# Optimization experiments

Measured on AMD Instinct MI355X. Metric: run time of the kernel, lower is better.

The kernel has to match this reference:

```python
import jax, jax.numpy as jnp
import numpy as np

# dims: P planes, N planar nodes/plane, M nexus nodes, E edges/plane, C classes
P, N, M, E, C, FP, FN = 3, 100000, 30000, 200000, 5, 64, 32


def class_linear(x, W, b):
    # x: [..., C, in], W: [C, out, in], b: [C, out] -> [..., C, out]
    return jnp.einsum('...ci,coi->...co', x, W) + b


def setup_inputs() -> dict:
    key = jax.random.key(0)
    ks = jax.random.split(key, 12)
    def nrm(k, shape, scale=1.0):
        return jax.random.normal(k, shape, jnp.float32) * scale
    return {
        'x': nrm(ks[0], (P, N, C, FP)),
        'nexus': nrm(ks[1], (M, C, FN)),
        'edge_src': jax.random.randint(ks[2], (P, E), 0, N, jnp.int32),
        'edge_dst': jax.random.randint(ks[3], (P, E), 0, M, jnp.int32),
        'Wn1': nrm(ks[4], (C, FN, P * FP), (P * FP) ** -0.5),
        'bn1': jnp.zeros((C, FN), jnp.float32),
        'Wn2': nrm(ks[5], (C, FN, FN), FN ** -0.5),
        'bn2': jnp.zeros((C, FN), jnp.float32),
        'We': nrm(ks[6], (P, C, 1, FP + FN), (FP + FN) ** -0.5),
        'be': jnp.zeros((P, C, 1), jnp.float32),
        'Wd1': nrm(ks[7], (P, C, FP, FP + FN), (FP + FN) ** -0.5),
        'bd1': jnp.zeros((P, C, FP), jnp.float32),
        'Wd2': nrm(ks[8], (P, C, FP, FP), FP ** -0.5),
        'bd2': jnp.zeros((P, C, FP), jnp.float32),
    }


def reference(x, nexus, edge_src, edge_dst, Wn1, bn1, Wn2, bn2,
              We, be, Wd1, bd1, Wd2, bd2):
    # --- nexus_up: SimpleConv (sum-aggregate planar features at nexus nodes) ---
    def up_one(xp, src, dst):
        return jax.ops.segment_sum(xp[src], dst, num_segments=M)  # [M,C,FP]
    up = jax.vmap(up_one)(x, edge_src, edge_dst)                   # [P,M,C,FP]
    # torch.cat(n, dim=-1) over planes -> [M, C, P*FP]
    n_cat = jnp.transpose(up, (1, 2, 0, 3)).reshape(M, C, P * FP)

    # --- nexus_net: ClassLinear -> tanh -> ClassLinear -> tanh ---
    n = jnp.tanh(class_linear(n_cat, Wn1, bn1))
    n = jnp.tanh(class_linear(n, Wn2, bn2))                        # [M,C,FN]

    # --- nexus_down per plane (flow target_to_source, aggr mean at src) ---
    def down_one(xp, src, dst, We_p, be_p, W1, b1, W2, b2):
        x_i = xp[src]                                              # [E,C,FP]
        n_j = n[dst]                                               # [E,C,FN]
        feat = jax.lax.stop_gradient(jnp.concatenate([x_i, n_j], -1))
        # per-class scalar logit, softmax over class dim (dim=1)
        w = jax.nn.softmax(class_linear(feat, We_p, be_p), axis=1)  # [E,C,1]
        msg = w * n_j                                               # [E,C,FN]
        s = jax.ops.segment_sum(msg, src, num_segments=N)           # [N,C,FN]
        cnt = jax.ops.segment_sum(jnp.ones((E,), msg.dtype), src, num_segments=N)
        aggr = s / jnp.maximum(cnt, 1.0)[:, None, None]             # scatter-mean
        h = jnp.tanh(class_linear(jnp.concatenate([xp, aggr], -1), W1, b1))
        return jnp.tanh(class_linear(h, W2, b2))                    # [N,C,FP]

    out = jax.vmap(down_one)(x, edge_src, edge_dst, We, be, Wd1, bd1, Wd2, bd2)
    return out  # [P,N,C,FP] updated planar embeddings (x['u'],x['v'],x['y'])
```

## Files before the change

### kernel.cpp

```cpp
#include <hip/hip_runtime.h>
#include <hip/hip_fp16.h>

#define P_ 3
#define N_ 100000
#define M_ 30000
#define E_ 200000
#define C_ 5
#define FP_ 64
#define FN_ 32
#define PFP_ 192
#define FPFN_ 96
#define PE_ 600000
#define PN_ 300000
#define PM_ 90000
#define NT_ 32
#define XSP_ 324
#define TILES_ ((N_ + NT_ - 1) / NT_)
#define NTD_ 64
#define TILESD_ ((N_ + NTD_ - 1) / NTD_)
#define CFN_ 160
#define NW1_ 92160
#define NW2_ 61440
#define NB_S_ ((PN_ + 1023) / 1024)
#define NB_D_ ((PM_ + 1023) / 1024)
#define NB_CNT_ ((PE_ + 255) / 256)
#define NB_WC_ ((NW1_ + 255) / 256)
#define NB_PROJ_ (P_ * TILES_)
#define NB_FILL_ ((PE_ + 319) / 320)

typedef _Float16 f16x8 __attribute__((ext_vector_type(8)));
typedef float f32x4 __attribute__((ext_vector_type(4)));

__device__ __forceinline__ float fast_tanh(float v) {
  float x = fminf(fmaxf(v, -15.0f), 15.0f);
  float t = __expf(2.0f * x);
  return __fdividef(t - 1.0f, t + 1.0f);
}

__device__ __forceinline__ f16x8 ld8(const __half* p) {
  return *(const f16x8*)(const void*)p;
}

__global__ void k_countw(const int* __restrict__ esrc, const int* __restrict__ edst,
                         int* __restrict__ cnt_src, int* __restrict__ cnt_dst,
                         const float* __restrict__ Wd1, const float* __restrict__ Wd2,
                         __half* __restrict__ w1h, __half* __restrict__ w2h) {
  int b = blockIdx.x;
  if (b < NB_CNT_) {
    int i = b * 256 + threadIdx.x;
    if (i >= PE_) return;
    int p = i / E_;
    atomicAdd(&cnt_src[p * N_ + esrc[i]], 1);
    atomicAdd(&cnt_dst[p * M_ + edst[i]], 1);
  } else {
    int i = (b - NB_CNT_) * 256 + threadIdx.x;
    if (i < NW1_) w1h[i] = __float2half(Wd1[i]);
    if (i < NW2_) w2h[i] = __float2half(Wd2[i]);
  }
}

__global__ void k_scan1c(const int* __restrict__ in_s, int* __restrict__ out_s,
                         int* __restrict__ aux_s,
                         const int* __restrict__ in_d, int* __restrict__ out_d,
                         int* __restrict__ aux_d) {
  __shared__ int lds[256];
  int b = blockIdx.x, t = threadIdx.x;
  const int* in;
  int* out;
  int* aux;
  int n;
  if (b < NB_S_) { in = in_s; out = out_s; aux = aux_s; n = PN_; }
  else           { b -= NB_S_; in = in_d; out = out_d; aux = aux_d; n = PM_; }
  int base = b * 1024 + t * 4;
  int v0 = (base + 0 < n) ? in[base + 0] : 0;
  int v1 = (base + 1 < n) ? in[base + 1] : 0;
  int v2 = (base + 2 < n) ? in[base + 2] : 0;
  int v3 = (base + 3 < n) ? in[base + 3] : 0;
  lds[t] = v0 + v1 + v2 + v3;
  __syncthreads();
  for (int off = 1; off < 256; off <<= 1) {
    int xv = (t >= off) ? lds[t - off] : 0;
    __syncthreads();
    lds[t] += xv;
    __syncthreads();
  }
  if (t == 255) aux[b] = lds[255];
  int run = (t == 0) ? 0 : lds[t - 1];
  if (base + 0 < n) out[base + 0] = run; run += v0;
  if (base + 1 < n) out[base + 1] = run; run += v1;
  if (base + 2 < n) out[base + 2] = run; run += v2;
  if (base + 3 < n) out[base + 3] = run;
}

__global__ void k_scan2c(int* __restrict__ aux_s, int* __restrict__ end_s,
                         int* __restrict__ aux_d, int* __restrict__ end_d) {
  __shared__ int lds[1024];
  int t = threadIdx.x;
  int* aux = (blockIdx.x == 0) ? aux_s : aux_d;
  int* offe = (blockIdx.x == 0) ? end_s : end_d;
  int nb = (blockIdx.x == 0) ? NB_S_ : NB_D_;
  lds[t] = (t < nb) ? aux[t] : 0;
  __syncthreads();
  for (int off = 1; off < 1024; off <<= 1) {
    int xv = (t >= off) ? lds[t - off] : 0;
    __syncthreads();
    lds[t] += xv;
    __syncthreads();
  }
  if (t < nb) aux[t] = (t == 0) ? 0 : lds[t - 1];
  if (t == 0) offe[0] = lds[nb - 1];
}

__global__ void k_scan3c(int* __restrict__ off_s, const int* __restrict__ aux_s,
                         int* __restrict__ cur_s,
                         int* __restrict__ off_d, const int* __restrict__ aux_d,
                         int* __restrict__ cur_d) {
  int i = blockIdx.x * 256 + threadIdx.x;
  if (i < PN_) {
    int v = off_s[i] + aux_s[i >> 10];
    off_s[i] = v;
    cur_s[i] = v;
  } else if (i < PN_ + PM_) {
    int j = i - PN_;
    int v = off_d[j] + aux_d[j >> 10];
    off_d[j] = v;
    cur_d[j] = v;
  }
}

__global__ __launch_bounds__(320) void k_projfill(
    const float* __restrict__ x, const float* __restrict__ Wn1,
    const float* __restrict__ We,
    __half* __restrict__ y, float* __restrict__ xdot,
    __half* __restrict__ xh, int write_xh,
    const int* __restrict__ esrc, const int* __restrict__ edst,
    int* __restrict__ cur_src, int* __restrict__ cur_dst,
    int* __restrict__ list_src, int* __restrict__ list_src_e,
    int* __restrict__ list_dst, int* __restrict__ list_dst_e) {
  __shared__ __align__(16) __half xs[NT_ * XSP_];
  int bp = blockIdx.x;
  int t = threadIdx.x;

  if (bp >= NB_PROJ_) {
    int i = (bp - NB_PROJ_) * 320 + t;
    if (i < PE_) {
      int p = i / E_;
      int s = esrc[i], d = edst[i];
      int ps = atomicAdd(&cur_src[p * N_ + s], 1);
      list_src[ps] = d;
      list_src_e[ps] = i;
      int pd = atomicAdd(&cur_dst[p * M_ + d], 1);
      list_dst[pd] = s;
      list_dst_e[pd] = i;
    }
    return;
  }

  int p = bp / TILES_, tile = bp % TILES_;
  int base = tile * NT_;
  int rows = min(NT_, N_ - base);
  int g = t / CFN_, u = t % CFN_;
  int c = u >> 5;

  __half2 w[32];
  {
    const float* wr = &Wn1[(size_t)u * PFP_ + p * FP_];
    #pragma unroll
    for (int i = 0; i < 32; ++i) w[i] = __floats2half2_rn(wr[2*i], wr[2*i+1]);
  }

  const float* xb = x + (size_t)(p * N_ + base) * 320;
  __half* xo = xh + (size_t)(p * N_ + base) * 320;
  int chunks = rows * 40;
  for (int idx = t; idx < chunks; idx += 320) {
    int row = idx / 40, col = idx % 40;
    const float4* s4 = (const float4*)&xb[row * 320 + col * 8];
    float4 v0 = s4[0], v1 = s4[1];
    union { __half2 h[4]; float4 f; } u4;
    u4.h[0] = __floats2half2_rn(v0.x, v0.y);
    u4.h[1] = __floats2half2_rn(v0.z, v0.w);
    u4.h[2] = __floats2half2_rn(v1.x, v1.y);
    u4.h[3] = __floats2half2_rn(v1.z, v1.w);
    __half2* d = (__half2*)&xs[row * XSP_ + col * 8];
    d[0] = u4.h[0]; d[1] = u4.h[1]; d[2] = u4.h[2]; d[3] = u4.h[3];
    if (write_xh) *(float4*)&xo[row * 320 + col * 8] = u4.f;
  }
  __syncthreads();

  for (int r = g; r < rows; r += 2) {
    const __half2* xr = (const __half2*)&xs[r * XSP_ + c * FP_];
    __half2 acc = __floats2half2_rn(0.f, 0.f);
    #pragma unroll
    for (int i = 0; i < 32; ++i) acc = __hfma2(xr[i], w[i], acc);
    float s = __low2float(acc) + __high2float(acc);
    y[(size_t)(p * N_ + base + r) * CFN_ + u] = __float2half(s);
  }

  {
    int cx = t >> 6, nodex = t & 63;
    if (nodex < rows) {
      const __half2* xr = (const __half2*)&xs[nodex * XSP_ + cx * FP_];
      const float2* wer = (const float2*)&We[(p * C_ + cx) * FPFN_];
      float s = 0.f;
      #pragma unroll
      for (int i = 0; i < 32; ++i) {
        float2 wv = wer[i];
        __half2 xv = xr[i];
        s += __low2float(xv) * wv.x + __high2float(xv) * wv.y;
      }
      xdot[(size_t)(p * N_ + base + nodex) * C_ + cx] = s;
    }
  }
}

__global__ __launch_bounds__(320) void k_nexus(
    const __half* __restrict__ y,
    const int* __restrict__ off_dst, const int* __restrict__ list_dst,
    const int* __restrict__ list_dst_e, const int* __restrict__ esrc,
    const float* __restrict__ bn1,
    const float* __restrict__ Wn2, const float* __restrict__ bn2,
    const float* __restrict__ We,
    const float* __restrict__ xdot, const float* __restrict__ be,
    __half* __restrict__ nout, __half* __restrict__ wbuf) {
  __shared__ float part[4][CFN_];
  __shared__ __align__(16) float h1S[CFN_];
  __shared__ __align__(16) float h2S[CFN_];
  __shared__ float ndS[P_ * C_];
  __shared__ float beS[P_ * C_];
  int m = blockIdx.x;
  int t = threadIdx.x;
  int g = t / 80, u2 = t % 80;

  float afx = 0.f, afy = 0.f;
  #pragma unroll
  for (int p = 0; p < P_; ++p) {
    int o0 = off_dst[p * M_ + m];
    int o1 = off_dst[p * M_ + m + 1];
    const __half2* yp2 = (const __half2*)(y + (size_t)p * N_ * CFN_);
    for (int e0 = o0 + g; e0 < o1; e0 += 8) {
      int e1 = e0 + 4;
      int s0 = list_dst[e0];
      int s1 = list_dst[e1 < o1 ? e1 : e0];
      __half2 v0 = yp2[(size_t)s0 * 80 + u2];
      __half2 v1 = yp2[(size_t)s1 * 80 + u2];
      afx += __low2float(v0); afy += __high2float(v0);
      if (e1 < o1) { afx += __low2float(v1); afy += __high2float(v1); }
    }
  }
  part[g][2 * u2]     = afx;
  part[g][2 * u2 + 1] = afy;
  __syncthreads();
  if (t < CFN_) {
    float pre = part[0][t] + part[1][t] + part[2][t] + part[3][t] + bn1[t];
    h1S[t] = fast_tanh(pre);
  }
  __syncthreads();
  if (t < CFN_) {
    int c = t >> 5;
    const float4* f4 = (const float4*)&h1S[c * FN_];
    const float4* w4 = (const float4*)&Wn2[(size_t)t * FN_];
    float a = bn2[t];
    #pragma unroll
    for (int i = 0; i < FN_ / 4; ++i) {
      float4 f = f4[i], wv = w4[i];
      a += f.x * wv.x + f.y * wv.y + f.z * wv.z + f.w * wv.w;
    }
    float nv = fast_tanh(a);
    h2S[t] = nv;
    nout[(size_t)m * CFN_ + t] = __float2half(nv);
  }
  __syncthreads();
  if (t < P_ * C_) {
    int p = t / C_, cc = t % C_;
    const float* wv = &We[(p * C_ + cc) * FPFN_ + FP_];
    float a = 0.f;
    #pragma unroll
    for (int j = 0; j < FN_; ++j) a += h2S[cc * FN_ + j] * wv[j];
    ndS[t] = a;
    beS[t] = be[t];
  }
  __syncthreads();
  #pragma unroll
  for (int p = 0; p < P_; ++p) {
    int o0 = off_dst[p * M_ + m];
    int o1 = off_dst[p * M_ + m + 1];
    for (int e = o0 + t; e < o1; e += 320) {
      int i = list_dst_e[e];
      int src = esrc[i];
      const float* xd = &xdot[(size_t)(p * N_ + src) * C_];
      float lg[C_];
      #pragma unroll
      for (int cc = 0; cc < C_; ++cc) lg[cc] = xd[cc] + ndS[p * C_ + cc] + beS[p * C_ + cc];
      float mx = fmaxf(fmaxf(fmaxf(lg[0], lg[1]), fmaxf(lg[2], lg[3])), lg[4]);
      float s = 0.f;
      #pragma unroll
      for (int cc = 0; cc < C_; ++cc) { lg[cc] = __expf(lg[cc] - mx); s += lg[cc]; }
      float inv = __fdividef(1.0f, s);
      __half* wp = &wbuf[(size_t)i * C_];
      #pragma unroll
      for (int cc = 0; cc < C_; ++cc) wp[cc] = __float2half(lg[cc] * inv);
    }
  }
}

template<int XH>
__global__ __launch_bounds__(128, 6) void k_dec(
    const float* __restrict__ x, const __half* __restrict__ xh,
    const __half* __restrict__ nout, const __half* __restrict__ wbuf,
    const int* __restrict__ off_src, const int* __restrict__ list_src,
    const int* __restrict__ list_src_e,
    const __half* __restrict__ w1h, const float* __restrict__ bd1,
    const __half* __restrict__ w2h, const float* __restrict__ bd2,
    float* __restrict__ out) {
  __shared__ __align__(16) __half featS[NTD_ * 104];

  int bp = blockIdx.x;
  int pc = bp / TILESD_;
  int tile = bp % TILESD_;
  int p = pc / C_, c = pc % C_;
  int base = tile * NTD_;
  int rows = min(NTD_, N_ - base);

  int t = threadIdx.x;
  int w = t >> 6, l = t & 63;
  int l15 = l & 15, l4 = l >> 4;

  if constexpr (XH) {
    for (int idx = t; idx < NTD_ * 8; idx += 128) {
      int node = idx >> 3, q = idx & 7;
      if (node < rows) {
        float4 v = *(const float4*)&xh[(size_t)(p * N_ + base + node) * 320 + c * 64 + q * 8];
        *(float4*)&featS[node * 104 + q * 8] = v;
      }
    }
  } else {
    for (int idx = t; idx < NTD_ * 16; idx += 128) {
      int node = idx >> 4, fq = idx & 15;
      if (node < rows) {
        float4 v = *(const float4*)&x[(size_t)(p * N_ + base + node) * 320 + c * 64 + fq * 4];
        __half2* dst = (__half2*)&featS[node * 104 + fq * 4];
        dst[0] = __floats2half2_rn(v.x, v.y);
        dst[1] = __floats2half2_rn(v.z, v.w);
      }
    }
  }
  {
    int nd = t >> 1, hf = t & 1;
    if (nd < rows) {
      int pn = p * N_ + base + nd;
      int o0 = off_src[pn], o1 = off_src[pn + 1];
      float acc[16];
      #pragma unroll
      for (int i = 0; i < 16; ++i) acc[i] = 0.f;
      for (int e = o0; e < o1; e += 2) {
        int e1 = e + 1;
        bool has1 = (e1 < o1);
        int d0 = list_src[e];
        int i0 = list_src_e[e];
        int d1 = list_src[has1 ? e1 : e];
        int i1 = list_src_e[has1 ? e1 : e];
        float wg0 = __half2float(wbuf[(size_t)i0 * C_ + c]);
        float wg1 = __half2float(wbuf[(size_t)i1 * C_ + c]);
        const __half2* nr0 = (const __half2*)&nout[(size_t)d0 * CFN_ + c * FN_ + hf * 16];
        const __half2* nr1 = (const __half2*)&nout[(size_t)d1 * CFN_ + c * FN_ + hf * 16];
        __half2 v0[8], v1[8];
        #pragma unroll
        for (int i = 0; i < 8; ++i) v0[i] = nr0[i];
        #pragma unroll
        for (int i = 0; i < 8; ++i) v1[i] = nr1[i];
        #pragma unroll
        for (int i = 0; i < 8; ++i) {
          acc[2 * i]     += wg0 * __low2float(v0[i]);
          acc[2 * i + 1] += wg0 * __high2float(v0[i]);
        }
        if (has1) {
          #pragma unroll
          for (int i = 0; i < 8; ++i) {
            acc[2 * i]     += wg1 * __low2float(v1[i]);
            acc[2 * i + 1] += wg1 * __high2float(v1[i]);
          }
        }
      }
      float invd = __fdividef(1.0f, fmaxf((float)(o1 - o0), 1.0f));
      __half2* dst2 = (__half2*)&featS[nd * 104 + 64 + hf * 16];
      #pragma unroll
      for (int i = 0; i < 8; ++i)
        dst2[i] = __floats2half2_rn(acc[2 * i] * invd, acc[2 * i + 1] * invd);
    }
  }
  __syncthreads();

  int rbase = w * 32;
  const __half* w1g = w1h + (size_t)(p * C_ + c) * 64 * 96;
  const __half* w2g = w2h + (size_t)(p * C_ + c) * 64 * 64;

  f32x4 acc[2][4];
  #pragma unroll
  for (int tt = 0; tt < 4; ++tt) {
    float bv = bd1[(p * C_ + c) * FP_ + tt * 16 + l15];
    #pragma unroll
    for (int rt = 0; rt < 2; ++rt) acc[rt][tt] = (f32x4){bv, bv, bv, bv};
  }
  #pragma unroll
  for (int s = 0; s < 3; ++s) {
    f16x8 a0 = ld8(&featS[(rbase + l15) * 104 + s * 32 + l4 * 8]);
    f16x8 a1 = ld8(&featS[(rbase + 16 + l15) * 104 + s * 32 + l4 * 8]);
    #pragma unroll
    for (int tt = 0; tt < 4; ++tt) {
      f16x8 b = ld8(&w1g[(tt * 16 + l15) * 96 + s * 32 + l4 * 8]);
      acc[0][tt] = __builtin_amdgcn_mfma_f32_16x16x32_f16(a0, b, acc[0][tt], 0, 0, 0);
      acc[1][tt] = __builtin_amdgcn_mfma_f32_16x16x32_f16(a1, b, acc[1][tt], 0, 0, 0);
    }
  }
  #pragma unroll
  for (int rt = 0; rt < 2; ++rt)
    #pragma unroll
    for (int tt = 0; tt < 4; ++tt) {
      #pragma unroll
      for (int r = 0; r < 4; ++r) {
        int nrow = rbase + rt * 16 + l4 * 4 + r;
        featS[nrow * 104 + tt * 16 + l15] = __float2half(fast_tanh(acc[rt][tt][r]));
      }
    }

  f32x4 acc2[2][4];
  #pragma unroll
  for (int tt = 0; tt < 4; ++tt) {
    float bv = bd2[(p * C_ + c) * FP_ + tt * 16 + l15];
    #pragma unroll
    for (int rt = 0; rt < 2; ++rt) acc2[rt][tt] = (f32x4){bv, bv, bv, bv};
  }
  #pragma unroll
  for (int s = 0; s < 2; ++s) {
    f16x8 a0 = ld8(&featS[(rbase + l15) * 104 + s * 32 + l4 * 8]);
    f16x8 a1 = ld8(&featS[(rbase + 16 + l15) * 104 + s * 32 + l4 * 8]);
    #pragma unroll
    for (int tt = 0; tt < 4; ++tt) {
      f16x8 b = ld8(&w2g[(tt * 16 + l15) * 64 + s * 32 + l4 * 8]);
      acc2[0][tt] = __builtin_amdgcn_mfma_f32_16x16x32_f16(a0, b, acc2[0][tt], 0, 0, 0);
      acc2[1][tt] = __builtin_amdgcn_mfma_f32_16x16x32_f16(a1, b, acc2[1][tt], 0, 0, 0);
    }
  }
  #pragma unroll
  for (int rt = 0; rt < 2; ++rt)
    #pragma unroll
    for (int tt = 0; tt < 4; ++tt) {
      #pragma unroll
      for (int r = 0; r < 4; ++r) {
        int nrow = rbase + rt * 16 + l4 * 4 + r;
        int node = base + nrow;
        if (node < N_) {
          out[(size_t)(p * N_ + node) * 320 + c * 64 + tt * 16 + l15] =
              fast_tanh(acc2[rt][tt][r]);
        }
      }
    }
}

#define WS_Y      0ll
#define WS_NOUT   24000000ll
#define WS_LISTSE 26400000ll
#define WS_WBUF   27000000ll
#define WS_XDOT   28800000ll
#define WS_OFFS   30750000ll
#define WS_OFFD   31050001ll
#define WS_CURS   31140002ll
#define WS_CURD   31440002ll
#define WS_LISTS  31530002ll
#define WS_LISTD  32130002ll
#define WS_AUX1   32730002ll
#define WS_AUX2   32730514ll
#define WS_W1H    32731026ll
#define WS_W2H    32777106ll
#define WS_LISTDE 32808000ll
#define WS_XH     33408000ll
#define WS_XH_END_BYTES ((WS_XH + 48000000ll) * 4ll)

extern "C" void kernel_launch(void* const* d_in, const int* in_sizes, int n_in,
                              void* d_out, int out_size, void* d_ws, size_t ws_size,
                              hipStream_t stream) {
  const float* x   = (const float*)d_in[0];
  const int* esrc  = (const int*)d_in[2];
  const int* edst  = (const int*)d_in[3];
  const float* Wn1 = (const float*)d_in[4];
  const float* bn1 = (const float*)d_in[5];
  const float* Wn2 = (const float*)d_in[6];
  const float* bn2 = (const float*)d_in[7];
  const float* We  = (const float*)d_in[8];
  const float* be  = (const float*)d_in[9];
  const float* Wd1 = (const float*)d_in[10];
  const float* bd1 = (const float*)d_in[11];
  const float* Wd2 = (const float*)d_in[12];
  const float* bd2 = (const float*)d_in[13];
  float* out = (float*)d_out;

  float* wsf = (float*)d_ws;
  int*   wsi = (int*)d_ws;
  __half* ybuf = (__half*)d_ws;
  __half* nout = (__half*)(wsi + WS_NOUT);
  __half* wbuf = (__half*)(wsi + WS_WBUF);
  float* xdot = wsf + WS_XDOT;
  int* off_src = wsi + WS_OFFS;
  int* off_dst = wsi + WS_OFFD;
  int* cur_src = wsi + WS_CURS;
  int* cur_dst = wsi + WS_CURD;
  int* list_src = wsi + WS_LISTS;
  int* list_src_e = wsi + WS_LISTSE;
  int* list_dst = wsi + WS_LISTD;
  int* list_dst_e = wsi + WS_LISTDE;
  int* aux1 = wsi + WS_AUX1;
  int* aux2 = wsi + WS_AUX2;
  __half* w1h = (__half*)(wsi + WS_W1H);
  __half* w2h = (__half*)(wsi + WS_W2H);
  __half* xh  = (__half*)(wsi + WS_XH);

  int use_xh = (ws_size >= (size_t)WS_XH_END_BYTES) ? 1 : 0;

  hipMemsetAsync(cur_src, 0, (PN_ + PM_) * sizeof(int), stream);
  k_countw<<<NB_CNT_ + NB_WC_, 256, 0, stream>>>(esrc, edst, cur_src, cur_dst,
                                                 Wd1, Wd2, w1h, w2h);
  k_scan1c<<<NB_S_ + NB_D_, 256, 0, stream>>>(cur_src, off_src, aux1,
                                              cur_dst, off_dst, aux2);
  k_scan2c<<<2, 1024, 0, stream>>>(aux1, off_src + PN_, aux2, off_dst + PM_);
  k_scan3c<<<(PN_ + PM_ + 255) / 256, 256, 0, stream>>>(off_src, aux1, cur_src,
                                                        off_dst, aux2, cur_dst);

  k_projfill<<<NB_PROJ_ + NB_FILL_, 320, 0, stream>>>(
      x, Wn1, We, ybuf, xdot, xh, use_xh,
      esrc, edst, cur_src, cur_dst,
      list_src, list_src_e, list_dst, list_dst_e);

  k_nexus<<<M_, 320, 0, stream>>>(ybuf, off_dst, list_dst, list_dst_e, esrc,
                                  bn1, Wn2, bn2, We, xdot, be, nout, wbuf);

  if (use_xh) {
    k_dec<1><<<P_ * C_ * TILESD_, 128, 0, stream>>>(x, xh, nout, wbuf,
                                                    off_src, list_src, list_src_e,
                                                    w1h, bd1, w2h, bd2, out);
  } else {
    k_dec<0><<<P_ * C_ * TILESD_, 128, 0, stream>>>(x, xh, nout, wbuf,
                                                    off_src, list_src, list_src_e,
                                                    w1h, bd1, w2h, bd2, out);
  }
}
```

Before: 868.0 us.

## Use MFMA for nexus input projection with swizzled LDS tile and fp16 Wn1

Replaces the per-thread packed-half dot products in the projection kernel with 16x16x32 fp16 MFMA instructions. The tile grows to 64 nodes with 256 threads, and the LDS tile switches from a padded stride to an XOR swizzle. Wn1 is pre-converted to fp16 in the weight-conversion kernel so MFMA can load B fragments directly. The aim is to cut VALU work and register pressure in the projection and to gain fp32 accumulation. The cost is a new workspace region and a shift of the xh workspace offset.

```diff
diff --git a/kernel.cpp b/kernel.cpp
--- a/kernel.cpp
+++ b/kernel.cpp
@@ -13,20 +13,20 @@
 #define PE_ 600000
 #define PN_ 300000
 #define PM_ 90000
-#define NT_ 32
-#define XSP_ 324
+#define NT_ 64
 #define TILES_ ((N_ + NT_ - 1) / NT_)
 #define NTD_ 64
 #define TILESD_ ((N_ + NTD_ - 1) / NTD_)
 #define CFN_ 160
 #define NW1_ 92160
 #define NW2_ 61440
+#define NWN1_ 30720
 #define NB_S_ ((PN_ + 1023) / 1024)
 #define NB_D_ ((PM_ + 1023) / 1024)
 #define NB_CNT_ ((PE_ + 255) / 256)
 #define NB_WC_ ((NW1_ + 255) / 256)
 #define NB_PROJ_ (P_ * TILES_)
-#define NB_FILL_ ((PE_ + 319) / 320)
+#define NB_FILL_ ((PE_ + 255) / 256)
 
 typedef _Float16 f16x8 __attribute__((ext_vector_type(8)));
 typedef float f32x4 __attribute__((ext_vector_type(4)));
@@ -44,7 +44,9 @@
 __global__ void k_countw(const int* __restrict__ esrc, const int* __restrict__ edst,
                          int* __restrict__ cnt_src, int* __restrict__ cnt_dst,
                          const float* __restrict__ Wd1, const float* __restrict__ Wd2,
-                         __half* __restrict__ w1h, __half* __restrict__ w2h) {
+                         const float* __restrict__ Wn1,
+                         __half* __restrict__ w1h, __half* __restrict__ w2h,
+                         __half* __restrict__ wn1h) {
   int b = blockIdx.x;
   if (b < NB_CNT_) {
     int i = b * 256 + threadIdx.x;
@@ -56,6 +58,7 @@
     int i = (b - NB_CNT_) * 256 + threadIdx.x;
     if (i < NW1_) w1h[i] = __float2half(Wd1[i]);
     if (i < NW2_) w2h[i] = __float2half(Wd2[i]);
+    if (i < NWN1_) wn1h[i] = __float2half(Wn1[i]);
   }
 }
 
@@ -128,8 +131,8 @@
   }
 }
 
-__global__ __launch_bounds__(320) void k_projfill(
-    const float* __restrict__ x, const float* __restrict__ Wn1,
+__global__ __launch_bounds__(256) void k_projfill(
+    const float* __restrict__ x, const __half* __restrict__ wn1h,
     const float* __restrict__ We,
     __half* __restrict__ y, float* __restrict__ xdot,
     __half* __restrict__ xh, int write_xh,
@@ -137,12 +140,12 @@
     int* __restrict__ cur_src, int* __restrict__ cur_dst,
     int* __restrict__ list_src, int* __restrict__ list_src_e,
     int* __restrict__ list_dst, int* __restrict__ list_dst_e) {
-  __shared__ __align__(16) __half xs[NT_ * XSP_];
+  __shared__ __align__(16) __half xs[NT_ * 320];
   int bp = blockIdx.x;
   int t = threadIdx.x;
 
   if (bp >= NB_PROJ_) {
-    int i = (bp - NB_PROJ_) * 320 + t;
+    int i = (bp - NB_PROJ_) * 256 + t;
     if (i < PE_) {
       int p = i / E_;
       int s = esrc[i], d = edst[i];
@@ -159,20 +162,10 @@
   int p = bp / TILES_, tile = bp % TILES_;
   int base = tile * NT_;
   int rows = min(NT_, N_ - base);
-  int g = t / CFN_, u = t % CFN_;
-  int c = u >> 5;
-
-  __half2 w[32];
-  {
-    const float* wr = &Wn1[(size_t)u * PFP_ + p * FP_];
-    #pragma unroll
-    for (int i = 0; i < 32; ++i) w[i] = __floats2half2_rn(wr[2*i], wr[2*i+1]);
-  }
 
   const float* xb = x + (size_t)(p * N_ + base) * 320;
   __half* xo = xh + (size_t)(p * N_ + base) * 320;
-  int chunks = rows * 40;
-  for (int idx = t; idx < chunks; idx += 320) {
+  for (int idx = t; idx < rows * 40; idx += 256) {
     int row = idx / 40, col = idx % 40;
     const float4* s4 = (const float4*)&xb[row * 320 + col * 8];
     float4 v0 = s4[0], v1 = s4[1];
@@ -181,31 +174,48 @@
     u4.h[1] = __floats2half2_rn(v0.z, v0.w);
     u4.h[2] = __floats2half2_rn(v1.x, v1.y);
     u4.h[3] = __floats2half2_rn(v1.z, v1.w);
-    __half2* d = (__half2*)&xs[row * XSP_ + col * 8];
-    d[0] = u4.h[0]; d[1] = u4.h[1]; d[2] = u4.h[2]; d[3] = u4.h[3];
+    *(float4*)&xs[row * 320 + ((col * 8) ^ ((row & 7) << 3))] = u4.f;
     if (write_xh) *(float4*)&xo[row * 320 + col * 8] = u4.f;
   }
   __syncthreads();
 
-  for (int r = g; r < rows; r += 2) {
-    const __half2* xr = (const __half2*)&xs[r * XSP_ + c * FP_];
-    __half2 acc = __floats2half2_rn(0.f, 0.f);
-    #pragma unroll
-    for (int i = 0; i < 32; ++i) acc = __hfma2(xr[i], w[i], acc);
-    float s = __low2float(acc) + __high2float(acc);
-    y[(size_t)(p * N_ + base + r) * CFN_ + u] = __float2half(s);
-  }
-
-  {
-    int cx = t >> 6, nodex = t & 63;
+  int w = t >> 6, l = t & 63;
+  int l15 = l & 15, l4 = l >> 4;
+  int nA = w * 16 + l15;
+  int swzA = (nA & 7) << 3;
+
+  #pragma unroll
+  for (int c = 0; c < C_; ++c) {
+    f16x8 a0 = ld8(&xs[nA * 320 + ((c * 64 + 0  + l4 * 8) ^ swzA)]);
+    f16x8 a1 = ld8(&xs[nA * 320 + ((c * 64 + 32 + l4 * 8) ^ swzA)]);
+    #pragma unroll
+    for (int ct = 0; ct < 2; ++ct) {
+      const __half* wb = &wn1h[(size_t)(c * 32 + ct * 16 + l15) * PFP_ + p * 64];
+      f16x8 b0 = ld8(&wb[0  + l4 * 8]);
+      f16x8 b1 = ld8(&wb[32 + l4 * 8]);
+      f32x4 acc = (f32x4){0.f, 0.f, 0.f, 0.f};
+      acc = __builtin_amdgcn_mfma_f32_16x16x32_f16(a0, b0, acc, 0, 0, 0);
+      acc = __builtin_amdgcn_mfma_f32_16x16x32_f16(a1, b1, acc, 0, 0, 0);
+      #pragma unroll
+      for (int r = 0; r < 4; ++r) {
+        int node = w * 16 + l4 * 4 + r;
+        if (node < rows)
+          y[(size_t)(p * N_ + base + node) * CFN_ + c * 32 + ct * 16 + l15] =
+              __float2half(acc[r]);
+      }
+    }
+  }
+
+  for (int idx = t; idx < C_ * NT_; idx += 256) {
+    int cx = idx >> 6, nodex = idx & 63;
     if (nodex < rows) {
-      const __half2* xr = (const __half2*)&xs[nodex * XSP_ + cx * FP_];
+      int swz = (nodex & 7) << 3;
       const float2* wer = (const float2*)&We[(p * C_ + cx) * FPFN_];
       float s = 0.f;
       #pragma unroll
       for (int i = 0; i < 32; ++i) {
+        __half2 xv = *(const __half2*)&xs[nodex * 320 + ((cx * 64 + 2 * i) ^ swz)];
         float2 wv = wer[i];
-        __half2 xv = xr[i];
         s += __low2float(xv) * wv.x + __high2float(xv) * wv.y;
       }
       xdot[(size_t)(p * N_ + base + nodex) * C_ + cx] = s;
@@ -473,7 +483,8 @@
 #define WS_W1H    32731026ll
 #define WS_W2H    32777106ll
 #define WS_LISTDE 32808000ll
-#define WS_XH     33408000ll
+#define WS_WN1H   33408000ll
+#define WS_XH     33423360ll
 #define WS_XH_END_BYTES ((WS_XH + 48000000ll) * 4ll)
 
 extern "C" void kernel_launch(void* const* d_in, const int* in_sizes, int n_in,
@@ -512,21 +523,22 @@
   int* aux2 = wsi + WS_AUX2;
   __half* w1h = (__half*)(wsi + WS_W1H);
   __half* w2h = (__half*)(wsi + WS_W2H);
+  __half* wn1h = (__half*)(wsi + WS_WN1H);
   __half* xh  = (__half*)(wsi + WS_XH);
 
   int use_xh = (ws_size >= (size_t)WS_XH_END_BYTES) ? 1 : 0;
 
   hipMemsetAsync(cur_src, 0, (PN_ + PM_) * sizeof(int), stream);
   k_countw<<<NB_CNT_ + NB_WC_, 256, 0, stream>>>(esrc, edst, cur_src, cur_dst,
-                                                 Wd1, Wd2, w1h, w2h);
+                                                 Wd1, Wd2, Wn1, w1h, w2h, wn1h);
   k_scan1c<<<NB_S_ + NB_D_, 256, 0, stream>>>(cur_src, off_src, aux1,
                                               cur_dst, off_dst, aux2);
   k_scan2c<<<2, 1024, 0, stream>>>(aux1, off_src + PN_, aux2, off_dst + PM_);
   k_scan3c<<<(PN_ + PM_ + 255) / 256, 256, 0, stream>>>(off_src, aux1, cur_src,
                                                         off_dst, aux2, cur_dst);
 
-  k_projfill<<<NB_PROJ_ + NB_FILL_, 320, 0, stream>>>(
-      x, Wn1, We, ybuf, xdot, xh, use_xh,
+  k_projfill<<<NB_PROJ_ + NB_FILL_, 256, 0, stream>>>(
+      x, wn1h, We, ybuf, xdot, xh, use_xh,
       esrc, edst, cur_src, cur_dst,
       list_src, list_src_e, list_dst, list_dst_e);
 
```

New measurement: 795.5 us. -8.4%, faster.
